# Optimization experiments

Measured on AMD Instinct MI355X. Metric: run time of the kernel, lower is better.

The kernel has to match this reference:

```python
import jax, jax.numpy as jnp
import numpy as np
from jax import lax

B, J, C, K, TOK, CH, H = 2048, 17, 480, 3, 64, 960, 6
HD = C // H  # 80
EPS = 1e-5

def gelu(x):
    return jax.nn.gelu(x, approximate=False)

def layernorm(x, g, b):
    mu = jnp.mean(x, axis=-1, keepdims=True)
    var = jnp.var(x, axis=-1, keepdims=True)
    return (x - mu) * lax.rsqrt(var + EPS) * g + b

def groupnorm(x, g, b, groups=16):
    # x: (B, C, J) -> normalize over (C//groups * J) per group
    n, c, j = x.shape
    xg = x.reshape(n, groups, -1)
    mu = jnp.mean(xg, axis=-1, keepdims=True)
    var = jnp.var(xg, axis=-1, keepdims=True)
    xg = (xg - mu) * lax.rsqrt(var + EPS)
    return xg.reshape(n, c, j) * g[None, :, None] + b[None, :, None]

def dwconv1d(x, w, b, pad):
    # x: (B, C, J), w: (C, 1, Kw) depthwise
    y = lax.conv_general_dilated(x, w, window_strides=(1,), padding=[(pad, pad)],
                                 dimension_numbers=('NCH', 'OIH', 'NCH'),
                                 feature_group_count=x.shape[1])
    return y + b[None, :, None]

def setup_inputs() -> dict:
    key = jax.random.key(0)
    ks = jax.random.split(key, 16)
    n = jax.random.normal
    return {
        'x': n(ks[0], (B, J, C), dtype=jnp.float32),
        'adj': n(ks[1], (K, J, J), dtype=jnp.float32) * 0.1,
        'norm1_g': jnp.ones((J,), jnp.float32), 'norm1_b': jnp.zeros((J,), jnp.float32),
        'gcn1_w': n(ks[2], (C * K, C), jnp.float32) * 0.02, 'gcn1_b': jnp.zeros((C * K,), jnp.float32),
        'dw_w': n(ks[3], (C, 1, 7), jnp.float32) * 0.1, 'dw_b': jnp.zeros((C,), jnp.float32),
        'dwgn_g': jnp.ones((C,), jnp.float32), 'dwgn_b': jnp.zeros((C,), jnp.float32),
        'mlp1_w1': n(ks[4], (TOK, J), jnp.float32) * 0.02, 'mlp1_b1': jnp.zeros((TOK,), jnp.float32),
        'mlp1_w2': n(ks[5], (J, TOK), jnp.float32) * 0.02, 'mlp1_b2': jnp.zeros((J,), jnp.float32),
        'qkv_w': n(ks[6], (3 * C, C), jnp.float32) * 0.02, 'qkv_b': jnp.zeros((3 * C,), jnp.float32),
        'proj_w': n(ks[7], (C, C), jnp.float32) * 0.02, 'proj_b': jnp.zeros((C,), jnp.float32),
        'pos_w': n(ks[8], (C, 1, 9), jnp.float32) * 0.1, 'pos_b': jnp.zeros((C,), jnp.float32),
        'gnf_g': jnp.ones((C,), jnp.float32), 'gnf_b': jnp.zeros((C,), jnp.float32),
        'norm2_g': jnp.ones((C,), jnp.float32), 'norm2_b': jnp.zeros((C,), jnp.float32),
        'gcn2_w': n(ks[9], (C * K, C), jnp.float32) * 0.02, 'gcn2_b': jnp.zeros((C * K,), jnp.float32),
        'mlp2_w1': n(ks[10], (CH, C), jnp.float32) * 0.02, 'mlp2_b1': jnp.zeros((CH,), jnp.float32),
        'mlp2_w2': n(ks[11], (C, CH), jnp.float32) * 0.02, 'mlp2_b2': jnp.zeros((C,), jnp.float32),
    }

def reference(x, adj, norm1_g, norm1_b, gcn1_w, gcn1_b, dw_w, dw_b, dwgn_g, dwgn_b,
              mlp1_w1, mlp1_b1, mlp1_w2, mlp1_b2, qkv_w, qkv_b, proj_w, proj_b,
              pos_w, pos_b, gnf_g, gnf_b, norm2_g, norm2_b, gcn2_w, gcn2_b,
              mlp2_w1, mlp2_b1, mlp2_w2, mlp2_b2):
    b = x.shape[0]
    xc = jnp.transpose(x, (0, 2, 1))            # (b, c, j)
    res_spatial = xc
    xn = layernorm(xc, norm1_g, norm1_b)        # LN over joints
    # --- GCN branch 1: 1x1 conv then adjacency einsum ---
    y = jnp.einsum('bcj,oc->boj', xn, gcn1_w) + gcn1_b[None, :, None]
    y = y.reshape(b, K, C, J)
    x_gcn1 = jnp.einsum('bkcv,kvw->bcw', y, adj)  # (b, c, j)
    # --- depthwise conv + GN + GELU + token Mlp ---
    d = gelu(groupnorm(dwconv1d(xn, dw_w, dw_b, 3), dwgn_g, dwgn_b))
    x_mjem = gelu(d @ mlp1_w1.T + mlp1_b1) @ mlp1_w2.T + mlp1_b2  # mix over j
    # --- spatial global attention (6 heads over joints + dwconv pos) ---
    xt = jnp.transpose(xn, (0, 2, 1))           # (b, j, c)
    qkv = xt @ qkv_w.T + qkv_b                  # (b, j, 3c)
    qkv = qkv.reshape(b, J, 3, H, HD).transpose(2, 0, 3, 1, 4)  # (3, b, h, j, hd)
    q, k, v = qkv[0], qkv[1], qkv[2]
    attn = jax.nn.softmax(jnp.einsum('bhqd,bhkd->bhqk', q, k) * (HD ** -0.5), axis=-1)
    o = jnp.einsum('bhqk,bhkd->bhqd', attn, v).transpose(0, 2, 1, 3).reshape(b, J, C)
    o = o @ proj_w.T + proj_b
    x_gsa = jnp.transpose(o, (0, 2, 1)) + dwconv1d(xn, pos_w, pos_b, 4)  # (b, c, j)
    # --- fuse ---
    fused = groupnorm(x_gsa + x_gcn1 + x_mjem, gnf_g, gnf_b)
    xc = res_spatial + gelu(fused)
    # --- channel stage ---
    xj = jnp.transpose(xc, (0, 2, 1))           # (b, j, c)
    res_channel = xj
    xn2 = layernorm(xj, norm2_g, norm2_b)       # LN over channels
    xcc = jnp.transpose(xn2, (0, 2, 1))         # (b, c, j)
    y2 = jnp.einsum('bcj,oc->boj', xcc, gcn2_w) + gcn2_b[None, :, None]
    y2 = y2.reshape(b, K, C, J)
    x_gcn2 = jnp.transpose(jnp.einsum('bkcv,kvw->bcw', y2, adj), (0, 2, 1))  # (b, j, c)
    mlp_out = gelu(xn2 @ mlp2_w1.T + mlp2_b1) @ mlp2_w2.T + mlp2_b2
    # sca_block is undefined in the source __init__ -> identity
    return res_channel + mlp_out + x_gcn2
```

## Files before the change

### kernel.cpp

```cpp
#include <hip/hip_runtime.h>
#include <hip/hip_bf16.h>

#define DI __device__ __forceinline__

typedef __attribute__((ext_vector_type(8))) short bf16x8;
typedef __attribute__((ext_vector_type(4))) float f32x4;

namespace {
constexpr int B_ = 2048, J_ = 17, C_ = 480, K_ = 3, TOK_ = 64, CH_ = 960, H_ = 6, HD_ = 80;
constexpr int C3_ = 3 * C_;
constexpr float EPSF = 1e-5f;
}

DI float gelu_f(float x) {
  const float kA2 = 2.f * 0.7978845608028654f;
  const float kB2 = 2.f * 0.7978845608028654f * 0.044715f;
  const float z = fmaf(-kB2 * x, x * x, -kA2 * x);
  return x / (1.f + __expf(z));
}
DI float b2f(__hip_bfloat16 v) { return __bfloat162float(v); }
DI __hip_bfloat16 f2b(float v) { return __float2bfloat16(v); }
DI float s2f(short s) { return __uint_as_float(((unsigned)(unsigned short)s) << 16); }
DI unsigned pk2(float a, float b) {
  union { unsigned u; __hip_bfloat16 h[2]; } p;
  p.h[0] = f2b(a); p.h[1] = f2b(b);
  return p.u;
}

DI void gl16(const void* g, void* l) {
  __builtin_amdgcn_global_load_lds(
      (const __attribute__((address_space(1))) unsigned int*)g,
      (__attribute__((address_space(3))) unsigned int*)l, 16, 0, 0);
}

__global__ __launch_bounds__(256) void cvt_all_kernel(
    const float* __restrict__ s0, const float* __restrict__ s1,
    const float* __restrict__ s2, const float* __restrict__ s3,
    const float* __restrict__ s4, const float* __restrict__ s5,
    __hip_bfloat16* __restrict__ d) {
  constexpr int SG = C3_ * C_;
  constexpr int O1 = SG, O2 = 2 * SG, O3 = 3 * SG;
  constexpr int O4 = O3 + C_ * C_;
  constexpr int O5 = O4 + CH_ * C_;
  const int i = (blockIdx.x * 256 + threadIdx.x) * 4;
  const float* s; int off;
  if      (i < O1) { s = s0; off = i; }
  else if (i < O2) { s = s1; off = i - O1; }
  else if (i < O3) { s = s2; off = i - O2; }
  else if (i < O4) { s = s3; off = i - O3; }
  else if (i < O5) { s = s4; off = i - O4; }
  else             { s = s5; off = i - O5; }
  const float4 v = *reinterpret_cast<const float4*>(s + off);
  union { ushort4 u; __hip_bfloat16 h[4]; } o;
  o.h[0] = f2b(v.x); o.h[1] = f2b(v.y); o.h[2] = f2b(v.z); o.h[3] = f2b(v.w);
  *reinterpret_cast<ushort4*>(reinterpret_cast<unsigned short*>(d) + i) = o.u;
}

__global__ __launch_bounds__(256) void ln1_kernel(const float* __restrict__ x,
                                                  const float* __restrict__ g,
                                                  const float* __restrict__ bt,
                                                  __hip_bfloat16* __restrict__ xnT, int nBC) {
  const int t = blockIdx.x * 256 + threadIdx.x;
  if (t >= nBC) return;
  const int b = t / C_, c = t % C_;
  const float* xp = x + (size_t)b * J_ * C_ + c;
  float v[J_];
  float s = 0.f;
  #pragma unroll
  for (int j = 0; j < J_; ++j) { v[j] = xp[j * C_]; s += v[j]; }
  const float mu = s * (1.f / J_);
  float sq = 0.f;
  #pragma unroll
  for (int j = 0; j < J_; ++j) { const float d = v[j] - mu; sq += d * d; }
  const float rs = rsqrtf(sq * (1.f / J_) + EPSF);
  __hip_bfloat16* op = xnT + (size_t)b * J_ * C_ + c;
  #pragma unroll
  for (int j = 0; j < J_; ++j) op[j * C_] = f2b((v[j] - mu) * rs * g[j] + bt[j]);
}

template<int KD, int EPI>
__global__ __launch_bounds__(256) void gemm_lds(const __hip_bfloat16* __restrict__ A,
                                                const __hip_bfloat16* __restrict__ W,
                                                const float* __restrict__ bias,
                                                __hip_bfloat16* __restrict__ Dst, int Ntot,
                                                const __hip_bfloat16* __restrict__ r1,
                                                const __hip_bfloat16* __restrict__ r2,
                                                float* __restrict__ outf) {
  constexpr int NST = (KD + 63) / 64;
  constexpr bool TAIL = (KD % 64) != 0;
  constexpr int ROWB = KD * 2;
  __shared__ __align__(16) char smem[57344];

  const int lane = threadIdx.x & 63;
  const int wid  = threadIdx.x >> 6;
  const int m0g = blockIdx.x * 128;
  const int n0g = blockIdx.y * 96;

  const int srow = lane >> 3;
  const int scbs = ((lane & 7) * 16) ^ ((srow & 7) << 4);
  auto stage = [&](int t, int bi) {
    const int kb = t * 128;
    const int ab = bi * 16384;
    const int bb = 32768 + bi * 12288;
    #pragma unroll
    for (int i = wid; i < 16; i += 4) {
      const int r = i * 8 + srow;
      gl16((const char*)A + (size_t)(m0g + r) * ROWB + kb + scbs, smem + ab + i * 1024);
    }
    #pragma unroll
    for (int i = wid; i < 12; i += 4) {
      const int r = i * 8 + srow;
      gl16((const char*)W + (size_t)(n0g + r) * ROWB + kb + scbs, smem + bb + i * 1024);
    }
  };

  const f32x4 zf = {0.f, 0.f, 0.f, 0.f};
  f32x4 acc[4][3];
  #pragma unroll
  for (int mi = 0; mi < 4; ++mi)
    #pragma unroll
    for (int ni = 0; ni < 3; ++ni) acc[mi][ni] = zf;

  const int rA0 = (wid >> 1) * 64 + (lane & 15);
  const int rB0 = (wid & 1) * 48 + (lane & 15);
  const int swz = (lane & 7) << 4;
  const int kq  = (lane >> 4) * 16;

  stage(0, 0);
  __syncthreads();
  int buf = 0;
  for (int t = 0; t < NST; ++t) {
    if (t + 1 < NST) stage(t + 1, buf ^ 1);
    const int abase = buf * 16384;
    const int bbase = 32768 + buf * 12288;
    const int nks = (TAIL && t == NST - 1) ? 1 : 2;
    for (int ks = 0; ks < nks; ++ks) {
      const int cb = (ks * 64 + kq) ^ swz;
      bf16x8 av[4], bv[3];
      #pragma unroll
      for (int mi = 0; mi < 4; ++mi)
        av[mi] = *reinterpret_cast<const bf16x8*>(smem + abase + (rA0 + mi * 16) * 128 + cb);
      #pragma unroll
      for (int ni = 0; ni < 3; ++ni)
        bv[ni] = *reinterpret_cast<const bf16x8*>(smem + bbase + (rB0 + ni * 16) * 128 + cb);
      #pragma unroll
      for (int mi = 0; mi < 4; ++mi)
        #pragma unroll
        for (int ni = 0; ni < 3; ++ni)
          acc[mi][ni] = __builtin_amdgcn_mfma_f32_16x16x32_bf16(av[mi], bv[ni], acc[mi][ni], 0, 0, 0);
    }
    __syncthreads();
    buf ^= 1;
  }

  const int col0 = n0g + (wid & 1) * 48 + (lane & 15);
  const int r0   = m0g + (wid >> 1) * 64 + ((lane >> 4) << 2);
  #pragma unroll
  for (int ni = 0; ni < 3; ++ni) {
    const int col = col0 + ni * 16;
    const float bvv = bias[col];
    #pragma unroll
    for (int mi = 0; mi < 4; ++mi) {
      #pragma unroll
      for (int r = 0; r < 4; ++r) {
        const size_t idx = (size_t)(r0 + mi * 16 + r) * Ntot + col;
        float v = acc[mi][ni][r] + bvv;
        if (EPI == 1) v = gelu_f(v);
        if (EPI == 2) outf[idx] = v + b2f(r1[idx]) + b2f(r2[idx]);
        else Dst[idx] = f2b(v);
      }
    }
  }
}

__global__ __launch_bounds__(512) void attn_kernel(const __hip_bfloat16* __restrict__ qkv,
                                                   __hip_bfloat16* __restrict__ o) {
  constexpr int SROW = 1448;
  const int b = blockIdx.x, tid = threadIdx.x;
  __shared__ __align__(16) __hip_bfloat16 sqkv[J_ * SROW];
  __shared__ float S[H_][J_][J_];
  {
    const uint4* src = (const uint4*)(qkv + (size_t)b * J_ * C3_);
    uint4* dst = (uint4*)&sqkv[0];
    for (int i = tid; i < 3060; i += 512) {
      const int j = i / 180, u = i - j * 180;
      dst[j * 181 + u] = src[i];
    }
  }
  __syncthreads();
  for (int i = tid; i < H_ * J_ * J_; i += 512) {
    const int h = i / (J_ * J_), r = i % (J_ * J_), qj = r / J_, kj = r % J_;
    const bf16x8* qp = (const bf16x8*)&sqkv[qj * SROW + h * HD_];
    const bf16x8* kp = (const bf16x8*)&sqkv[kj * SROW + C_ + h * HD_];
    float acc = 0.f;
    #pragma unroll
    for (int d8 = 0; d8 < HD_ / 8; ++d8) {
      const bf16x8 qv = qp[d8], kv = kp[d8];
      #pragma unroll
      for (int t = 0; t < 8; ++t) acc += s2f(qv[t]) * s2f(kv[t]);
    }
    S[h][i % (J_ * J_) / J_][kj] = acc * 0.11180339887498949f;
  }
  __syncthreads();
  if (tid < H_ * J_) {
    const int h = tid / J_, qj = tid % J_;
    float* row = S[h][qj];
    float m = row[0];
    #pragma unroll
    for (int kk = 1; kk < J_; ++kk) m = fmaxf(m, row[kk]);
    float s = 0.f;
    #pragma unroll
    for (int kk = 0; kk < J_; ++kk) { const float e = __expf(row[kk] - m); row[kk] = e; s += e; }
    const float inv = 1.f / s;
    #pragma unroll
    for (int kk = 0; kk < J_; ++kk) row[kk] *= inv;
  }
  __syncthreads();
  __hip_bfloat16* ob = o + (size_t)b * J_ * C_;
  for (int i = tid; i < J_ * C_; i += 512) {
    const int qj = i / C_, c = i % C_;
    const int h = c / HD_;
    const float* srow = S[h][qj];
    float acc = 0.f;
    #pragma unroll
    for (int kk = 0; kk < J_; ++kk) acc += srow[kk] * b2f(sqkv[kk * SROW + 2 * C_ + c]);
    ob[i] = f2b(acc);
  }
}

__global__ __launch_bounds__(512) void gcn_contract_kernel(const __hip_bfloat16* __restrict__ y,
                                                           const float* __restrict__ adj,
                                                           __hip_bfloat16* __restrict__ g) {
  const int b = blockIdx.x, tid = threadIdx.x;
  __shared__ float adjl[K_ * J_ * J_];
  for (int i = tid; i < K_ * J_ * J_; i += 512) adjl[i] = adj[i];
  __syncthreads();
  const int c = tid;
  if (c < C_) {
    float yv[K_][J_];
    const __hip_bfloat16* yb = y + (size_t)b * J_ * C3_ + c;
    #pragma unroll
    for (int k = 0; k < K_; ++k)
      #pragma unroll
      for (int v = 0; v < J_; ++v)
        yv[k][v] = b2f(yb[(size_t)v * C3_ + k * C_]);
    __hip_bfloat16* gp = g + (size_t)b * J_ * C_ + c;
    #pragma unroll
    for (int w = 0; w < J_; ++w) {
      float acc = 0.f;
      #pragma unroll
      for (int k = 0; k < K_; ++k)
        #pragma unroll
        for (int v = 0; v < J_; ++v)
          acc += yv[k][v] * adjl[(k * J_ + v) * J_ + w];
      gp[w * C_] = f2b(acc);
    }
  }
}

__global__ __launch_bounds__(512) void dwmlp_kernel(const __hip_bfloat16* __restrict__ xnT,
    const float* __restrict__ dww, const float* __restrict__ dwb,
    const float* __restrict__ gg, const float* __restrict__ gb,
    const float* __restrict__ w1, const float* __restrict__ b1,
    const float* __restrict__ w2, const float* __restrict__ b2,
    __hip_bfloat16* __restrict__ mjem) {
  __shared__ __align__(16) char lds[66560];
  __shared__ float gstat[16][2];
  constexpr int XL = 0, DT = 18432, W1P = 56832, W2P = 61952;
  const int b = blockIdx.x, tid = threadIdx.x;
  const int lane = tid & 63, wid = tid >> 6;

  {
    const uint4* src = (const uint4*)(xnT + (size_t)b * J_ * C_);
    uint4* dst = (uint4*)(lds + XL);
    for (int i = tid; i < 1020; i += 512) dst[i] = src[i];
  }
  {
    __hip_bfloat16* wp = (__hip_bfloat16*)(lds + W1P);
    const int t = tid >> 3, j0 = (tid & 7) * 5;
    #pragma unroll
    for (int e = 0; e < 5; ++e) {
      const int j = j0 + e;
      wp[t * 40 + j] = (j < J_) ? f2b(w1[t * J_ + j]) : f2b(0.f);
    }
  }
  if (tid < 256) {
    __hip_bfloat16* wp = (__hip_bfloat16*)(lds + W2P);
    const int j = tid >> 3, t0 = (tid & 7) * 9;
    #pragma unroll
    for (int e = 0; e < 9; ++e) {
      const int t = t0 + e;
      wp[j * 72 + t] = (j < J_ && t < TOK_) ? f2b(w2[j * TOK_ + t]) : f2b(0.f);
    }
  }
  if (tid < 32) gstat[tid >> 1][tid & 1] = 0.f;
  __syncthreads();

  const int c = tid;
  float dv[J_];
  if (c < C_) {
    const __hip_bfloat16* xl = (const __hip_bfloat16*)(lds + XL);
    float wv[7];
    #pragma unroll
    for (int t = 0; t < 7; ++t) wv[t] = dww[c * 7 + t];
    const float bias = dwb[c];
    float s = 0.f, sqs = 0.f;
    #pragma unroll
    for (int j = 0; j < J_; ++j) {
      float acc = bias;
      #pragma unroll
      for (int t = 0; t < 7; ++t) {
        const int jj = j - 3 + t;
        if (jj >= 0 && jj < J_) acc += b2f(xl[jj * C_ + c]) * wv[t];
      }
      dv[j] = acc; s += acc; sqs += acc * acc;
    }
    atomicAdd(&gstat[c / 30][0], s);
    atomicAdd(&gstat[c / 30][1], sqs);
  }
  __syncthreads();
  if (c < C_) {
    const float mu = gstat[c / 30][0] * (1.f / 510.f);
    const float var = gstat[c / 30][1] * (1.f / 510.f) - mu * mu;
    const float rs = rsqrtf(var + EPSF);
    const float sc = gg[c], of = gb[c];
    #pragma unroll
    for (int j = 0; j < J_; ++j) dv[j] = gelu_f((dv[j] - mu) * rs * sc + of);
    uint4* rp = (uint4*)(lds + DT + c * 80);
    uint4 q0, q1, q2;
    q0.x = pk2(dv[0], dv[1]);  q0.y = pk2(dv[2], dv[3]);
    q0.z = pk2(dv[4], dv[5]);  q0.w = pk2(dv[6], dv[7]);
    q1.x = pk2(dv[8], dv[9]);  q1.y = pk2(dv[10], dv[11]);
    q1.z = pk2(dv[12], dv[13]); q1.w = pk2(dv[14], dv[15]);
    q2.x = pk2(dv[16], 0.f);   q2.y = 0u; q2.z = 0u; q2.w = 0u;
    const uint4 zq = {0u, 0u, 0u, 0u};
    rp[0] = q0; rp[1] = q1; rp[2] = q2; rp[3] = zq; rp[4] = zq;
  }
  __syncthreads();

  const int lr = lane & 15, kc = lane >> 4;
  bf16x8 a1[4];
  #pragma unroll
  for (int mi = 0; mi < 4; ++mi)
    a1[mi] = *(const bf16x8*)(lds + W1P + (lr + mi * 16) * 80 + kc * 16);
  bf16x8 a2[2][2];
  #pragma unroll
  for (int mi = 0; mi < 2; ++mi)
    #pragma unroll
    for (int kk = 0; kk < 2; ++kk)
      a2[mi][kk] = *(const bf16x8*)(lds + W2P + (lr + mi * 16) * 144 + kk * 64 + kc * 16);
  float b1v[4][4];
  #pragma unroll
  for (int mi = 0; mi < 4; ++mi)
    #pragma unroll
    for (int r = 0; r < 4; ++r) b1v[mi][r] = b1[mi * 16 + kc * 4 + r];
  float b2v[4];
  #pragma unroll
  for (int r = 0; r < 4; ++r) b2v[r] = b2[kc * 4 + r];
  const float b2v16 = b2[16];

  char* hs = lds + XL + wid * 2304;
  const f32x4 zf4 = {0.f, 0.f, 0.f, 0.f};
  for (int cb = wid; cb < 30; cb += 8) {
    const int c0 = cb * 16;
    const bf16x8 bf = *(const bf16x8*)(lds + DT + (c0 + lr) * 80 + kc * 16);
    f32x4 acc1[4];
    #pragma unroll
    for (int mi = 0; mi < 4; ++mi)
      acc1[mi] = __builtin_amdgcn_mfma_f32_16x16x32_bf16(a1[mi], bf, zf4, 0, 0, 0);
    #pragma unroll
    for (int mi = 0; mi < 4; ++mi) {
      const float g0 = gelu_f(acc1[mi][0] + b1v[mi][0]);
      const float g1 = gelu_f(acc1[mi][1] + b1v[mi][1]);
      const float g2 = gelu_f(acc1[mi][2] + b1v[mi][2]);
      const float g3 = gelu_f(acc1[mi][3] + b1v[mi][3]);
      unsigned* hp = (unsigned*)(hs + lr * 144 + (mi * 16 + kc * 4) * 2);
      hp[0] = pk2(g0, g1);
      hp[1] = pk2(g2, g3);
    }
    f32x4 acc2[2] = {zf4, zf4};
    #pragma unroll
    for (int kk = 0; kk < 2; ++kk) {
      const bf16x8 hb = *(const bf16x8*)(hs + lr * 144 + kk * 64 + kc * 16);
      #pragma unroll
      for (int mi = 0; mi < 2; ++mi)
        acc2[mi] = __builtin_amdgcn_mfma_f32_16x16x32_bf16(a2[mi][kk], hb, acc2[mi], 0, 0, 0);
    }
    __hip_bfloat16* mp = mjem + (size_t)b * J_ * C_ + (c0 + lr);
    #pragma unroll
    for (int r = 0; r < 4; ++r)
      mp[(kc * 4 + r) * C_] = f2b(acc2[0][r] + b2v[r]);
    if (kc == 0) mp[16 * C_] = f2b(acc2[1][0] + b2v16);
  }
}

__global__ __launch_bounds__(512) void fuse_kernel(
    const float* __restrict__ x, const __hip_bfloat16* __restrict__ xnT,
    const __hip_bfloat16* __restrict__ g1o, const __hip_bfloat16* __restrict__ projo,
    const __hip_bfloat16* __restrict__ mjem,
    const float* __restrict__ posw, const float* __restrict__ posb,
    const float* __restrict__ gnfg, const float* __restrict__ gnfb,
    const float* __restrict__ n2g, const float* __restrict__ n2b,
    __hip_bfloat16* __restrict__ resch, __hip_bfloat16* __restrict__ xn2) {
  const int b = blockIdx.x, tid = threadIdx.x;
  __shared__ float xcl[J_][C_];
  __shared__ float gstat[16][2];
  __shared__ float lnst[J_][2];
  if (tid < 32) gstat[tid >> 1][tid & 1] = 0.f;
  __syncthreads();
  const int c = tid;
  float fz[J_];
  if (c < C_) {
    float xnv[J_];
    const __hip_bfloat16* xp = xnT + (size_t)b * J_ * C_ + c;
    #pragma unroll
    for (int j = 0; j < J_; ++j) xnv[j] = b2f(xp[j * C_]);
    float pw[9];
    #pragma unroll
    for (int t = 0; t < 9; ++t) pw[t] = posw[c * 9 + t];
    const float pb = posb[c];
    const __hip_bfloat16* pj = projo + (size_t)b * J_ * C_ + c;
    const __hip_bfloat16* mp = mjem + (size_t)b * J_ * C_ + c;
    const __hip_bfloat16* gp = g1o + (size_t)b * J_ * C_ + c;
    float s = 0.f, sqs = 0.f;
    #pragma unroll
    for (int j = 0; j < J_; ++j) {
      float pos = pb;
      #pragma unroll
      for (int t = 0; t < 9; ++t) {
        const int jj = j - 4 + t;
        if (jj >= 0 && jj < J_) pos += xnv[jj] * pw[t];
      }
      const float f = b2f(pj[j * C_]) + pos + b2f(gp[j * C_]) + b2f(mp[j * C_]);
      fz[j] = f; s += f; sqs += f * f;
    }
    atomicAdd(&gstat[c / 30][0], s);
    atomicAdd(&gstat[c / 30][1], sqs);
  }
  __syncthreads();
  if (c < C_) {
    const float mu = gstat[c / 30][0] * (1.f / 510.f);
    const float var = gstat[c / 30][1] * (1.f / 510.f) - mu * mu;
    const float rs = rsqrtf(var + EPSF);
    const float sc = gnfg[c], of = gnfb[c];
    const float* xr = x + (size_t)b * J_ * C_ + c;
    __hip_bfloat16* rp = resch + (size_t)b * J_ * C_ + c;
    #pragma unroll
    for (int j = 0; j < J_; ++j) {
      const float xcv = xr[j * C_] + gelu_f((fz[j] - mu) * rs * sc + of);
      xcl[j][c] = xcv;
      rp[j * C_] = f2b(xcv);
    }
  }
  __syncthreads();
  const int wid = tid >> 6, lane = tid & 63;
  for (int j = wid; j < J_; j += 8) {
    float ls = 0.f, lq = 0.f;
    for (int cc = lane; cc < C_; cc += 64) { const float v = xcl[j][cc]; ls += v; lq += v * v; }
    #pragma unroll
    for (int off = 32; off > 0; off >>= 1) { ls += __shfl_xor(ls, off); lq += __shfl_xor(lq, off); }
    if (lane == 0) {
      const float mu = ls * (1.f / C_);
      const float var = lq * (1.f / C_) - mu * mu;
      lnst[j][0] = mu; lnst[j][1] = rsqrtf(var + EPSF);
    }
  }
  __syncthreads();
  if (c < C_) {
    const float sc = n2g[c], of = n2b[c];
    __hip_bfloat16* xp2 = xn2 + (size_t)b * J_ * C_ + c;
    #pragma unroll
    for (int j = 0; j < J_; ++j)
      xp2[j * C_] = f2b((xcl[j][c] - lnst[j][0]) * lnst[j][1] * sc + of);
  }
}

extern "C" void kernel_launch(void* const* d_in, const int* in_sizes, int n_in,
                              void* d_out, int out_size, void* d_ws, size_t ws_size,
                              hipStream_t stream) {
  const float* x      = (const float*)d_in[0];
  const float* adj    = (const float*)d_in[1];
  const float* n1g    = (const float*)d_in[2];
  const float* n1b    = (const float*)d_in[3];
  const float* gcn1_w = (const float*)d_in[4];
  const float* gcn1_b = (const float*)d_in[5];
  const float* dw_w   = (const float*)d_in[6];
  const float* dw_b   = (const float*)d_in[7];
  const float* dwgn_g = (const float*)d_in[8];
  const float* dwgn_b = (const float*)d_in[9];
  const float* m1w1   = (const float*)d_in[10];
  const float* m1b1   = (const float*)d_in[11];
  const float* m1w2   = (const float*)d_in[12];
  const float* m1b2   = (const float*)d_in[13];
  const float* qkv_w  = (const float*)d_in[14];
  const float* qkv_b  = (const float*)d_in[15];
  const float* proj_w = (const float*)d_in[16];
  const float* proj_b = (const float*)d_in[17];
  const float* pos_w  = (const float*)d_in[18];
  const float* pos_b  = (const float*)d_in[19];
  const float* gnf_g  = (const float*)d_in[20];
  const float* gnf_b  = (const float*)d_in[21];
  const float* n2g    = (const float*)d_in[22];
  const float* n2b    = (const float*)d_in[23];
  const float* gcn2_w = (const float*)d_in[24];
  const float* gcn2_b = (const float*)d_in[25];
  const float* m2w1   = (const float*)d_in[26];
  const float* m2b1   = (const float*)d_in[27];
  const float* m2w2   = (const float*)d_in[28];
  const float* m2b2   = (const float*)d_in[29];
  float* out = (float*)d_out;
  char* ws = (char*)d_ws;
  (void)in_sizes; (void)n_in; (void)out_size;

  auto a256 = [](size_t b) { return (b + 255) & ~(size_t)255; };
  const size_t wbytes = 3 * a256((size_t)C3_ * C_ * 2) + a256((size_t)C_ * C_ * 2) +
                        a256((size_t)CH_ * C_ * 2) + a256((size_t)C_ * CH_ * 2);
  int nch = 16;
  for (int cand : {1, 2, 4, 8, 16}) {
    const size_t Mcb = (size_t)(B_ / cand) * J_;
    const size_t fp = wbytes + a256(Mcb * C3_ * 2) + 6 * a256(Mcb * C_ * 2);
    if (fp <= ws_size) { nch = cand; break; }
  }
  const int Bc = B_ / nch;
  const int Mc = Bc * J_;

  size_t off = 0;
  auto alloc = [&](size_t bytes) { char* p = ws + off; off += a256(bytes); return p; };
  __hip_bfloat16* w_qkv = (__hip_bfloat16*)alloc((size_t)C3_ * C_ * 2);
  __hip_bfloat16* w_g1  = (__hip_bfloat16*)alloc((size_t)C3_ * C_ * 2);
  __hip_bfloat16* w_g2  = (__hip_bfloat16*)alloc((size_t)C3_ * C_ * 2);
  __hip_bfloat16* w_pr  = (__hip_bfloat16*)alloc((size_t)C_ * C_ * 2);
  __hip_bfloat16* w_21  = (__hip_bfloat16*)alloc((size_t)CH_ * C_ * 2);
  __hip_bfloat16* w_22  = (__hip_bfloat16*)alloc((size_t)C_ * CH_ * 2);
  __hip_bfloat16* BIG   = (__hip_bfloat16*)alloc((size_t)Mc * C3_ * 2);
  __hip_bfloat16* xnT   = (__hip_bfloat16*)alloc((size_t)Mc * C_ * 2);
  __hip_bfloat16* attno = (__hip_bfloat16*)alloc((size_t)Mc * C_ * 2);
  __hip_bfloat16* projo = (__hip_bfloat16*)alloc((size_t)Mc * C_ * 2);
  __hip_bfloat16* mjem  = (__hip_bfloat16*)alloc((size_t)Mc * C_ * 2);
  __hip_bfloat16* g1o   = (__hip_bfloat16*)alloc((size_t)Mc * C_ * 2);
  __hip_bfloat16* resch = (__hip_bfloat16*)alloc((size_t)Mc * C_ * 2);
  __hip_bfloat16* xn2   = attno;
  __hip_bfloat16* g2o   = g1o;
  __hip_bfloat16* hbuf  = BIG;

  cvt_all_kernel<<<3150, 256, 0, stream>>>(qkv_w, gcn1_w, gcn2_w, proj_w, m2w1, m2w2, w_qkv);

  for (int ci = 0; ci < nch; ++ci) {
    const float* xc = x + (size_t)ci * Bc * J_ * C_;
    float* outc = out + (size_t)ci * Bc * J_ * C_;
    ln1_kernel<<<(Bc * C_ + 255) / 256, 256, 0, stream>>>(xc, n1g, n1b, xnT, Bc * C_);
    gemm_lds<C_, 0><<<dim3(Mc / 128, C3_ / 96), 256, 0, stream>>>(xnT, w_qkv, qkv_b, BIG, C3_, nullptr, nullptr, nullptr);
    attn_kernel<<<Bc, 512, 0, stream>>>(BIG, attno);
    gemm_lds<C_, 0><<<dim3(Mc / 128, C3_ / 96), 256, 0, stream>>>(xnT, w_g1, gcn1_b, BIG, C3_, nullptr, nullptr, nullptr);
    gcn_contract_kernel<<<Bc, 512, 0, stream>>>(BIG, adj, g1o);
    gemm_lds<C_, 0><<<dim3(Mc / 128, C_ / 96), 256, 0, stream>>>(attno, w_pr, proj_b, projo, C_, nullptr, nullptr, nullptr);
    dwmlp_kernel<<<Bc, 512, 0, stream>>>(xnT, dw_w, dw_b, dwgn_g, dwgn_b, m1w1, m1b1, m1w2, m1b2, mjem);
    fuse_kernel<<<Bc, 512, 0, stream>>>(xc, xnT, g1o, projo, mjem, pos_w, pos_b,
                                        gnf_g, gnf_b, n2g, n2b, resch, xn2);
    gemm_lds<C_, 0><<<dim3(Mc / 128, C3_ / 96), 256, 0, stream>>>(xn2, w_g2, gcn2_b, BIG, C3_, nullptr, nullptr, nullptr);
    gcn_contract_kernel<<<Bc, 512, 0, stream>>>(BIG, adj, g2o);
    gemm_lds<C_, 1><<<dim3(Mc / 128, CH_ / 96), 256, 0, stream>>>(xn2, w_21, m2b1, hbuf, CH_, nullptr, nullptr, nullptr);
    gemm_lds<CH_, 2><<<dim3(Mc / 128, C_ / 96), 256, 0, stream>>>(hbuf, w_22, m2b2, nullptr, C_, resch, g2o, outc);
  }
}
```

Measured before the change: 739.7 us.

## Split dwconv+MLP kernel into separate dwconv and MFMA MLP kernels

Splits the fused dwconv/groupnorm/token-MLP kernel, which used about 66KB of LDS, into two kernels. A dwconv kernel writes a padded per-channel bf16 intermediate to global memory, and a small-LDS, 256-thread MLP kernel processes 16 channel tiles per block. The MLP output moves to a channel-major layout of 20 elements per channel that the fuse kernel reads contiguously. This targets low occupancy from the large LDS footprint, at the cost of an extra kernel launch and a global round-trip for the intermediate.

```diff
diff --git a/kernel.cpp b/kernel.cpp
--- a/kernel.cpp
+++ b/kernel.cpp
@@ -199,7 +199,7 @@
       #pragma unroll
       for (int t = 0; t < 8; ++t) acc += s2f(qv[t]) * s2f(kv[t]);
     }
-    S[h][i % (J_ * J_) / J_][kj] = acc * 0.11180339887498949f;
+    S[h][qj][kj] = acc * 0.11180339887498949f;
   }
   __syncthreads();
   if (tid < H_ * J_) {
@@ -258,48 +258,26 @@
   }
 }
 
-__global__ __launch_bounds__(512) void dwmlp_kernel(const __hip_bfloat16* __restrict__ xnT,
+__global__ __launch_bounds__(512) void dwconv_kernel(const __hip_bfloat16* __restrict__ xnT,
     const float* __restrict__ dww, const float* __restrict__ dwb,
     const float* __restrict__ gg, const float* __restrict__ gb,
-    const float* __restrict__ w1, const float* __restrict__ b1,
-    const float* __restrict__ w2, const float* __restrict__ b2,
-    __hip_bfloat16* __restrict__ mjem) {
-  __shared__ __align__(16) char lds[66560];
+    __hip_bfloat16* __restrict__ dpr) {
+  __shared__ __align__(16) __hip_bfloat16 xl[J_ * C_];
   __shared__ float gstat[16][2];
-  constexpr int XL = 0, DT = 18432, W1P = 56832, W2P = 61952;
   const int b = blockIdx.x, tid = threadIdx.x;
-  const int lane = tid & 63, wid = tid >> 6;
-
   {
     const uint4* src = (const uint4*)(xnT + (size_t)b * J_ * C_);
-    uint4* dst = (uint4*)(lds + XL);
+    uint4* dst = (uint4*)&xl[0];
     for (int i = tid; i < 1020; i += 512) dst[i] = src[i];
   }
-  {
-    __hip_bfloat16* wp = (__hip_bfloat16*)(lds + W1P);
-    const int t = tid >> 3, j0 = (tid & 7) * 5;
-    #pragma unroll
-    for (int e = 0; e < 5; ++e) {
-      const int j = j0 + e;
-      wp[t * 40 + j] = (j < J_) ? f2b(w1[t * J_ + j]) : f2b(0.f);
-    }
-  }
-  if (tid < 256) {
-    __hip_bfloat16* wp = (__hip_bfloat16*)(lds + W2P);
-    const int j = tid >> 3, t0 = (tid & 7) * 9;
-    #pragma unroll
-    for (int e = 0; e < 9; ++e) {
-      const int t = t0 + e;
-      wp[j * 72 + t] = (j < J_ && t < TOK_) ? f2b(w2[j * TOK_ + t]) : f2b(0.f);
-    }
-  }
   if (tid < 32) gstat[tid >> 1][tid & 1] = 0.f;
   __syncthreads();
-
   const int c = tid;
   float dv[J_];
   if (c < C_) {
-    const __hip_bfloat16* xl = (const __hip_bfloat16*)(lds + XL);
+    float xv[J_];
+    #pragma unroll
+    for (int j = 0; j < J_; ++j) xv[j] = b2f(xl[j * C_ + c]);
     float wv[7];
     #pragma unroll
     for (int t = 0; t < 7; ++t) wv[t] = dww[c * 7 + t];
@@ -311,7 +289,7 @@
       #pragma unroll
       for (int t = 0; t < 7; ++t) {
         const int jj = j - 3 + t;
-        if (jj >= 0 && jj < J_) acc += b2f(xl[jj * C_ + c]) * wv[t];
+        if (jj >= 0 && jj < J_) acc = fmaf(xv[jj], wv[t], acc);
       }
       dv[j] = acc; s += acc; sqs += acc * acc;
     }
@@ -326,15 +304,43 @@
     const float sc = gg[c], of = gb[c];
     #pragma unroll
     for (int j = 0; j < J_; ++j) dv[j] = gelu_f((dv[j] - mu) * rs * sc + of);
-    uint4* rp = (uint4*)(lds + DT + c * 80);
     uint4 q0, q1, q2;
-    q0.x = pk2(dv[0], dv[1]);  q0.y = pk2(dv[2], dv[3]);
-    q0.z = pk2(dv[4], dv[5]);  q0.w = pk2(dv[6], dv[7]);
-    q1.x = pk2(dv[8], dv[9]);  q1.y = pk2(dv[10], dv[11]);
+    q0.x = pk2(dv[0], dv[1]);   q0.y = pk2(dv[2], dv[3]);
+    q0.z = pk2(dv[4], dv[5]);   q0.w = pk2(dv[6], dv[7]);
+    q1.x = pk2(dv[8], dv[9]);   q1.y = pk2(dv[10], dv[11]);
     q1.z = pk2(dv[12], dv[13]); q1.w = pk2(dv[14], dv[15]);
-    q2.x = pk2(dv[16], 0.f);   q2.y = 0u; q2.z = 0u; q2.w = 0u;
+    q2.x = pk2(dv[16], 0.f);    q2.y = 0u; q2.z = 0u; q2.w = 0u;
     const uint4 zq = {0u, 0u, 0u, 0u};
-    rp[0] = q0; rp[1] = q1; rp[2] = q2; rp[3] = zq; rp[4] = zq;
+    uint4* rp = (uint4*)(dpr + ((size_t)b * C_ + c) * 32);
+    rp[0] = q0; rp[1] = q1; rp[2] = q2; rp[3] = zq;
+  }
+}
+
+__global__ __launch_bounds__(256) void mlp_kernel(const __hip_bfloat16* __restrict__ dpr,
+    const float* __restrict__ w1, const float* __restrict__ b1,
+    const float* __restrict__ w2, const float* __restrict__ b2,
+    __hip_bfloat16* __restrict__ mjem_r) {
+  __shared__ __align__(16) char lds[18944];
+  constexpr int W1P = 0, W2P = 5120, HS = 9728;
+  const int tid = threadIdx.x, lane = tid & 63, wid = tid >> 6;
+
+  {
+    __hip_bfloat16* wp = (__hip_bfloat16*)(lds + W1P);
+    const int t = tid >> 2, j0 = (tid & 3) * 10;
+    #pragma unroll
+    for (int e = 0; e < 10; ++e) {
+      const int j = j0 + e;
+      wp[t * 40 + j] = (j < J_) ? f2b(w1[t * J_ + j]) : f2b(0.f);
+    }
+  }
+  {
+    __hip_bfloat16* wp = (__hip_bfloat16*)(lds + W2P);
+    const int j = tid >> 3, t0 = (tid & 7) * 9;
+    #pragma unroll
+    for (int e = 0; e < 9; ++e) {
+      const int t = t0 + e;
+      wp[j * 72 + t] = (j < J_ && t < TOK_) ? f2b(w2[j * TOK_ + t]) : f2b(0.f);
+    }
   }
   __syncthreads();
 
@@ -359,11 +365,14 @@
   for (int r = 0; r < 4; ++r) b2v[r] = b2[kc * 4 + r];
   const float b2v16 = b2[16];
 
-  char* hs = lds + XL + wid * 2304;
+  char* hs = lds + HS + wid * 2304;
   const f32x4 zf4 = {0.f, 0.f, 0.f, 0.f};
-  for (int cb = wid; cb < 30; cb += 8) {
-    const int c0 = cb * 16;
-    const bf16x8 bf = *(const bf16x8*)(lds + DT + (c0 + lr) * 80 + kc * 16);
+  #pragma unroll
+  for (int it = 0; it < 4; ++it) {
+    const int gcb = blockIdx.x * 16 + wid * 4 + it;
+    const int b = gcb / 30, cbl = gcb - b * 30;
+    const size_t row0 = (size_t)b * C_ + cbl * 16;
+    const bf16x8 bf = *(const bf16x8*)(dpr + (row0 + lr) * 32 + kc * 8);
     f32x4 acc1[4];
     #pragma unroll
     for (int mi = 0; mi < 4; ++mi)
@@ -386,18 +395,18 @@
       for (int mi = 0; mi < 2; ++mi)
         acc2[mi] = __builtin_amdgcn_mfma_f32_16x16x32_bf16(a2[mi][kk], hb, acc2[mi], 0, 0, 0);
     }
-    __hip_bfloat16* mp = mjem + (size_t)b * J_ * C_ + (c0 + lr);
+    __hip_bfloat16* mp = mjem_r + (row0 + lr) * 20;
     #pragma unroll
     for (int r = 0; r < 4; ++r)
-      mp[(kc * 4 + r) * C_] = f2b(acc2[0][r] + b2v[r]);
-    if (kc == 0) mp[16 * C_] = f2b(acc2[1][0] + b2v16);
+      mp[kc * 4 + r] = f2b(acc2[0][r] + b2v[r]);
+    if (kc == 0) mp[16] = f2b(acc2[1][0] + b2v16);
   }
 }
 
 __global__ __launch_bounds__(512) void fuse_kernel(
     const float* __restrict__ x, const __hip_bfloat16* __restrict__ xnT,
     const __hip_bfloat16* __restrict__ g1o, const __hip_bfloat16* __restrict__ projo,
-    const __hip_bfloat16* __restrict__ mjem,
+    const __hip_bfloat16* __restrict__ mjem_r,
     const float* __restrict__ posw, const float* __restrict__ posb,
     const float* __restrict__ gnfg, const float* __restrict__ gnfb,
     const float* __restrict__ n2g, const float* __restrict__ n2b,
@@ -420,7 +429,7 @@
     for (int t = 0; t < 9; ++t) pw[t] = posw[c * 9 + t];
     const float pb = posb[c];
     const __hip_bfloat16* pj = projo + (size_t)b * J_ * C_ + c;
-    const __hip_bfloat16* mp = mjem + (size_t)b * J_ * C_ + c;
+    const __hip_bfloat16* mp = mjem_r + ((size_t)b * C_ + c) * 20;
     const __hip_bfloat16* gp = g1o + (size_t)b * J_ * C_ + c;
     float s = 0.f, sqs = 0.f;
     #pragma unroll
@@ -431,7 +440,7 @@
         const int jj = j - 4 + t;
         if (jj >= 0 && jj < J_) pos += xnv[jj] * pw[t];
       }
-      const float f = b2f(pj[j * C_]) + pos + b2f(gp[j * C_]) + b2f(mp[j * C_]);
+      const float f = b2f(pj[j * C_]) + pos + b2f(gp[j * C_]) + b2f(mp[j]);
       fz[j] = f; s += f; sqs += f * f;
     }
     atomicAdd(&gstat[c / 30][0], s);
@@ -517,8 +526,10 @@
                         a256((size_t)CH_ * C_ * 2) + a256((size_t)C_ * CH_ * 2);
   int nch = 16;
   for (int cand : {1, 2, 4, 8, 16}) {
-    const size_t Mcb = (size_t)(B_ / cand) * J_;
-    const size_t fp = wbytes + a256(Mcb * C3_ * 2) + 6 * a256(Mcb * C_ * 2);
+    const size_t Bcb = (size_t)(B_ / cand);
+    const size_t Mcb = Bcb * J_;
+    const size_t fp = wbytes + a256(Mcb * C3_ * 2) + 5 * a256(Mcb * C_ * 2) +
+                      a256(Bcb * C_ * 20 * 2) + a256(Bcb * C_ * 32 * 2);
     if (fp <= ws_size) { nch = cand; break; }
   }
   const int Bc = B_ / nch;
@@ -536,9 +547,10 @@
   __hip_bfloat16* xnT   = (__hip_bfloat16*)alloc((size_t)Mc * C_ * 2);
   __hip_bfloat16* attno = (__hip_bfloat16*)alloc((size_t)Mc * C_ * 2);
   __hip_bfloat16* projo = (__hip_bfloat16*)alloc((size_t)Mc * C_ * 2);
-  __hip_bfloat16* mjem  = (__hip_bfloat16*)alloc((size_t)Mc * C_ * 2);
   __hip_bfloat16* g1o   = (__hip_bfloat16*)alloc((size_t)Mc * C_ * 2);
   __hip_bfloat16* resch = (__hip_bfloat16*)alloc((size_t)Mc * C_ * 2);
+  __hip_bfloat16* mjemr = (__hip_bfloat16*)alloc((size_t)Bc * C_ * 20 * 2);
+  __hip_bfloat16* dpr   = (__hip_bfloat16*)alloc((size_t)Bc * C_ * 32 * 2);
   __hip_bfloat16* xn2   = attno;
   __hip_bfloat16* g2o   = g1o;
   __hip_bfloat16* hbuf  = BIG;
@@ -554,8 +566,9 @@
     gemm_lds<C_, 0><<<dim3(Mc / 128, C3_ / 96), 256, 0, stream>>>(xnT, w_g1, gcn1_b, BIG, C3_, nullptr, nullptr, nullptr);
     gcn_contract_kernel<<<Bc, 512, 0, stream>>>(BIG, adj, g1o);
     gemm_lds<C_, 0><<<dim3(Mc / 128, C_ / 96), 256, 0, stream>>>(attno, w_pr, proj_b, projo, C_, nullptr, nullptr, nullptr);
-    dwmlp_kernel<<<Bc, 512, 0, stream>>>(xnT, dw_w, dw_b, dwgn_g, dwgn_b, m1w1, m1b1, m1w2, m1b2, mjem);
-    fuse_kernel<<<Bc, 512, 0, stream>>>(xc, xnT, g1o, projo, mjem, pos_w, pos_b,
+    dwconv_kernel<<<Bc, 512, 0, stream>>>(xnT, dw_w, dw_b, dwgn_g, dwgn_b, dpr);
+    mlp_kernel<<<Bc * 30 / 16, 256, 0, stream>>>(dpr, m1w1, m1b1, m1w2, m1b2, mjemr);
+    fuse_kernel<<<Bc, 512, 0, stream>>>(xc, xnT, g1o, projo, mjemr, pos_w, pos_b,
                                         gnf_g, gnf_b, n2g, n2b, resch, xn2);
     gemm_lds<C_, 0><<<dim3(Mc / 128, C3_ / 96), 256, 0, stream>>>(xn2, w_g2, gcn2_b, BIG, C3_, nullptr, nullptr, nullptr);
     gcn_contract_kernel<<<Bc, 512, 0, stream>>>(BIG, adj, g2o);
```

New measurement: 751.2 us. Within noise of the previous version (+1.6%).
